# Optimization experiments

Hardware: AMD Instinct MI355X
Metric: run time of the kernel (lower is better)

## Reference

```python
import jax, jax.numpy as jnp
import numpy as np

D_MODEL = 128
NUM_LAYERS = 2
D_FF = 512
VOCAB = 128
OUT_DIM = 10
B, S = 512, 256
EPS_FEAT = 1e-6
LN_EPS = 1e-5


def _pos_encoding(seq_len, d):
    pos = jnp.arange(seq_len, dtype=jnp.float32)[:, None]            # [S,1]
    div = jnp.exp(jnp.arange(0, d, 2, dtype=jnp.float32) * (-np.log(10000.0) / d))
    ang = pos * div                                                   # [S,D/2]
    pe = jnp.stack([jnp.sin(ang), jnp.cos(ang)], axis=-1).reshape(seq_len, d)
    return pe[:, None, :]                                             # [S,1,D]


def _layer_norm(x, g, b):
    mu = jnp.mean(x, axis=-1, keepdims=True)
    var = jnp.mean(jnp.square(x - mu), axis=-1, keepdims=True)
    return (x - mu) * jax.lax.rsqrt(var + LN_EPS) * g + b


def setup_inputs() -> dict:
    key = jax.random.key(0)
    ks = jax.random.split(key, 20)
    sc = 0.02
    inp = {
        'src': jax.random.randint(ks[0], (B, S), 0, VOCAB),
        'emb': jax.random.normal(ks[1], (VOCAB, D_MODEL), jnp.float32) * sc,
        'wq': jax.random.normal(ks[2], (NUM_LAYERS, D_MODEL, D_MODEL), jnp.float32) * sc,
        'bq': jnp.zeros((NUM_LAYERS, D_MODEL), jnp.float32),
        'wk': jax.random.normal(ks[3], (NUM_LAYERS, D_MODEL, D_MODEL), jnp.float32) * sc,
        'bk': jnp.zeros((NUM_LAYERS, D_MODEL), jnp.float32),
        'wv': jax.random.normal(ks[4], (NUM_LAYERS, D_MODEL, D_MODEL), jnp.float32) * sc,
        'bv': jnp.zeros((NUM_LAYERS, D_MODEL), jnp.float32),
        'w1': jax.random.normal(ks[5], (NUM_LAYERS, D_FF, D_MODEL), jnp.float32) * sc,
        'b1': jnp.zeros((NUM_LAYERS, D_FF), jnp.float32),
        'w2': jax.random.normal(ks[6], (NUM_LAYERS, D_MODEL, D_FF), jnp.float32) * sc,
        'b2': jnp.zeros((NUM_LAYERS, D_MODEL), jnp.float32),
        'g1': jnp.ones((NUM_LAYERS, D_MODEL), jnp.float32),
        'beta1': jnp.zeros((NUM_LAYERS, D_MODEL), jnp.float32),
        'g2': jnp.ones((NUM_LAYERS, D_MODEL), jnp.float32),
        'beta2': jnp.zeros((NUM_LAYERS, D_MODEL), jnp.float32),
        'fc_w': jax.random.normal(ks[7], (OUT_DIM, D_MODEL), jnp.float32) * sc,
        'fc_b': jnp.zeros((OUT_DIM,), jnp.float32),
    }
    return inp


def reference(src, emb, wq, bq, wk, bk, wv, bv, w1, b1, w2, b2,
              g1, beta1, g2, beta2, fc_w, fc_b):
    # src: [B,S] int -> permute -> [S,B]
    x = emb[src.T] * np.sqrt(float(D_MODEL))          # [S,B,D]
    x = x + _pos_encoding(x.shape[0], D_MODEL)
    for l in range(NUM_LAYERS):
        # Linear attention (faithful to original: einsum 'b' axis = seq here)
        Q = jax.nn.relu(jnp.einsum('sbd,ed->sbe', x, wq[l]) + bq[l]) + EPS_FEAT
        K = jax.nn.relu(jnp.einsum('sbd,ed->sbe', x, wk[l]) + bk[l]) + EPS_FEAT
        V = jnp.einsum('sbd,ed->sbe', x, wv[l]) + bv[l]
        KV = jnp.einsum('snd,sne->sde', K, V)         # [S,D,D] (n = batch axis)
        Z = 1.0 / (jnp.einsum('snd,sd->sn', Q, K.sum(axis=1)) + EPS_FEAT)  # [S,B]
        attn = jnp.einsum('snd,sde,sn->sne', Q, KV, Z)  # [S,B,D]
        x = _layer_norm(x + attn, g1[l], beta1[l])
        ff = jnp.einsum('sbf,df->sbd',
                        jax.nn.relu(jnp.einsum('sbd,fd->sbf', x, w1[l]) + b1[l]),
                        w2[l]) + b2[l]
        x = _layer_norm(x + ff, g2[l], beta2[l])
    x = jnp.transpose(x, (1, 0, 2))                   # [B,S,D]
    pooled = jnp.mean(x, axis=1)                      # [B,D]
    return pooled @ fc_w.T + fc_b                     # [B,OUT]
```

## Files before the change

kernel.cpp:

```cpp
#include <hip/hip_runtime.h>

typedef unsigned short u16;
typedef unsigned int u32;
typedef short bf16x8 __attribute__((ext_vector_type(8)));
typedef float f32x4 __attribute__((ext_vector_type(4)));

__device__ __forceinline__ float b2f(u16 v) { return __uint_as_float(((u32)v) << 16); }
__device__ __forceinline__ u16 f2b(float f) {
    u32 x = __float_as_uint(f);
    return (u16)((x + 0x7fffu + ((x >> 16) & 1u)) >> 16);
}
__device__ __forceinline__ float lo16(u32 w) { return __uint_as_float(w << 16); }
__device__ __forceinline__ float hi16(u32 w) { return __uint_as_float(w & 0xffff0000u); }

#define S_LEN 256
#define B_SZ  512
#define DM    128
#define DFF   512
#define MROWS (S_LEN * B_SZ)

__device__ __forceinline__ int sw16(int r, int d) {
    return r * 128 + ((((d >> 3) ^ (r & 15)) & 15) << 3) + (d & 7);
}

__global__ __launch_bounds__(256) void detect_kernel(const u32* __restrict__ embw,
                                                     int* __restrict__ flag) {
    int z = 0, big = 0;
    for (int i = threadIdx.x; i < 8192; i += 256) {
        u32 w = embw[i];
        u32 lo = w & 0xffffu;
        if (lo == 0u) z++;
        else if (((lo >> 7) & 0xffu) >= 0xC0u) big++;
    }
#pragma unroll
    for (int off = 32; off > 0; off >>= 1) {
        z   += __shfl_xor(z, off, 64);
        big += __shfl_xor(big, off, 64);
    }
    __shared__ int zz[4], bb[4];
    if ((threadIdx.x & 63) == 0) { zz[threadIdx.x >> 6] = z; bb[threadIdx.x >> 6] = big; }
    __syncthreads();
    if (threadIdx.x == 0) {
        int Z = zz[0] + zz[1] + zz[2] + zz[3];
        int Bc = bb[0] + bb[1] + bb[2] + bb[3];
        flag[0] = (Z > 4096 || Bc > 16) ? 1 : 0;
    }
}

struct Ptrs { const void* p[17]; };

__global__ __launch_bounds__(256) void convert_kernel(Ptrs ps, u16* __restrict__ canon,
                                                      const int* __restrict__ flag) {
    const int cnt[17] = {16384,32768,256,32768,256,32768,256,131072,1024,131072,
                         256,256,256,256,256,1280,10};
    const int off[17] = {0,16384,49152,49408,82176,82432,115200,115456,246528,
                         247552,378624,378880,379136,379392,379648,379904,381184};
    const int bst[18] = {0,8,24,25,41,42,58,59,123,124,188,189,190,191,192,193,194,195};
    const int isf = *flag;
    const int blk = blockIdx.x;
    int idx = 0;
#pragma unroll
    for (int i = 0; i < 17; ++i) if (blk >= bst[i + 1]) idx = i + 1;
    const int local = blk - bst[idx];
    const int n = cnt[idx];
    const void* sp = ps.p[idx];
    u16* dp = canon + off[idx];
#pragma unroll
    for (int j = 0; j < 8; ++j) {
        int e = local * 2048 + j * 256 + threadIdx.x;
        if (e < n) {
            u16 v = isf ? f2b(((const float*)sp)[e]) : ((const u16*)sp)[e];
            dp[e] = v;
        }
    }
}

__global__ __launch_bounds__(256) void embed_kernel(const int* __restrict__ src,
                                                    const u16* __restrict__ emb,
                                                    u16* __restrict__ X) {
    int idx = blockIdx.x * 256 + threadIdx.x;
    int d2 = idx & 63;
    int m = idx >> 6;
    int s = m >> 9;
    int b = m & 511;
    int tok = src[b * S_LEN + s];
    int d = d2 * 2;
    float e0 = b2f(emb[tok * DM + d])     * 11.3137084989847604f;
    float e1 = b2f(emb[tok * DM + d + 1]) * 11.3137084989847604f;
    float ang = (float)s * expf((float)d * -0.0719557841560639f);
    float v0 = e0 + sinf(ang);
    float v1 = e1 + cosf(ang);
    u32 w = (u32)f2b(v0) | ((u32)f2b(v1) << 16);
    *(u32*)(X + (size_t)m * DM + d) = w;
}

__global__ __launch_bounds__(256) void kvproj_kernel(
    const u16* __restrict__ X, const u16* __restrict__ Wk, const u16* __restrict__ bk,
    const u16* __restrict__ Wv, const u16* __restrict__ bv,
    u16* __restrict__ KVt, float* __restrict__ Ksum)
{
    __shared__ __align__(16) char sm_[49152];
    u16* Xs = (u16*)sm_;
    u16* Kt = (u16*)(sm_ + 16384);
    u16* Vt = (u16*)(sm_ + 32768);
    const int s = blockIdx.x, t = threadIdx.x;
    const int w = t >> 6, quad = (t >> 4) & 3, lr = t & 15;
    const u16* Xg = X + (size_t)s * B_SZ * DM;

    bf16x8 wkf[2][4], wvf[2][4];
    float kb[2], vb[2];
#pragma unroll
    for (int ct = 0; ct < 2; ++ct) {
        int e = w * 32 + ct * 16 + lr;
#pragma unroll
        for (int kc = 0; kc < 4; ++kc) {
            wkf[ct][kc] = *(const bf16x8*)(Wk + e * 128 + kc * 32 + quad * 8);
            wvf[ct][kc] = *(const bf16x8*)(Wv + e * 128 + kc * 32 + quad * 8);
        }
        kb[ct] = b2f(bk[e]);
        vb[ct] = b2f(bv[e]);
    }

    const f32x4 z4 = {0.f, 0.f, 0.f, 0.f};
    f32x4 kvacc[2][8];
#pragma unroll
    for (int dt = 0; dt < 2; ++dt)
#pragma unroll
        for (int ct = 0; ct < 8; ++ct) kvacc[dt][ct] = z4;
    float ks[2] = {0.f, 0.f};

    for (int b0 = 0; b0 < B_SZ; b0 += 64) {
        __syncthreads();
#pragma unroll
        for (int i = 0; i < 4; ++i) {
            int e8 = (i * 256 + t) * 8; int r = e8 >> 7, k0 = e8 & 127;
            *(uint4*)(Xs + sw16(r, k0)) = *(const uint4*)(Xg + (size_t)(b0 + r) * DM + k0);
        }
        __syncthreads();
        f32x4 pa[4][2];
#pragma unroll
        for (int mt = 0; mt < 4; ++mt) { pa[mt][0] = z4; pa[mt][1] = z4; }
#pragma unroll
        for (int kc = 0; kc < 4; ++kc) {
            bf16x8 a[4];
#pragma unroll
            for (int mt = 0; mt < 4; ++mt)
                a[mt] = *(const bf16x8*)(Xs + sw16(mt * 16 + lr, kc * 32 + quad * 8));
#pragma unroll
            for (int ct = 0; ct < 2; ++ct)
#pragma unroll
                for (int mt = 0; mt < 4; ++mt)
                    pa[mt][ct] = __builtin_amdgcn_mfma_f32_16x16x32_bf16(a[mt], wkf[ct][kc], pa[mt][ct], 0, 0, 0);
        }
#pragma unroll
        for (int ct = 0; ct < 2; ++ct) {
            int e = w * 32 + ct * 16 + lr, e7 = e & 7;
#pragma unroll
            for (int mt = 0; mt < 4; ++mt) {
                u16 h[4]; float ssum = 0.f;
#pragma unroll
                for (int j = 0; j < 4; ++j) {
                    float v = fmaxf(pa[mt][ct][j] + kb[ct], 0.f) + 1e-6f;
                    h[j] = f2b(v); ssum += b2f(h[j]);
                }
                ks[ct] += ssum;
                uint2 pk; pk.x = (u32)h[0] | ((u32)h[1] << 16); pk.y = (u32)h[2] | ((u32)h[3] << 16);
                int bs = mt * 2 + (quad >> 1);
                *(uint2*)(Kt + e * 64 + (((bs ^ e7) & 7) << 3) + (quad & 1) * 4) = pk;
            }
        }
#pragma unroll
        for (int mt = 0; mt < 4; ++mt) { pa[mt][0] = z4; pa[mt][1] = z4; }
#pragma unroll
        for (int kc = 0; kc < 4; ++kc) {
            bf16x8 a[4];
#pragma unroll
            for (int mt = 0; mt < 4; ++mt)
                a[mt] = *(const bf16x8*)(Xs + sw16(mt * 16 + lr, kc * 32 + quad * 8));
#pragma unroll
            for (int ct = 0; ct < 2; ++ct)
#pragma unroll
                for (int mt = 0; mt < 4; ++mt)
                    pa[mt][ct] = __builtin_amdgcn_mfma_f32_16x16x32_bf16(a[mt], wvf[ct][kc], pa[mt][ct], 0, 0, 0);
        }
#pragma unroll
        for (int ct = 0; ct < 2; ++ct) {
            int e = w * 32 + ct * 16 + lr, e7 = e & 7;
#pragma unroll
            for (int mt = 0; mt < 4; ++mt) {
                u16 h[4];
#pragma unroll
                for (int j = 0; j < 4; ++j) h[j] = f2b(pa[mt][ct][j] + vb[ct]);
                uint2 pk; pk.x = (u32)h[0] | ((u32)h[1] << 16); pk.y = (u32)h[2] | ((u32)h[3] << 16);
                int bs = mt * 2 + (quad >> 1);
                *(uint2*)(Vt + e * 64 + (((bs ^ e7) & 7) << 3) + (quad & 1) * 4) = pk;
            }
        }
        __syncthreads();
#pragma unroll
        for (int kc = 0; kc < 2; ++kc) {
            bf16x8 ka[2];
#pragma unroll
            for (int dt = 0; dt < 2; ++dt) {
                int d = (2 * w + dt) * 16 + lr;
                ka[dt] = *(const bf16x8*)(Kt + d * 64 + ((((kc * 4 + quad) ^ (d & 7)) & 7) << 3));
            }
#pragma unroll
            for (int ct = 0; ct < 8; ++ct) {
                int e = ct * 16 + lr;
                bf16x8 vf = *(const bf16x8*)(Vt + e * 64 + ((((kc * 4 + quad) ^ (e & 7)) & 7) << 3));
                kvacc[0][ct] = __builtin_amdgcn_mfma_f32_16x16x32_bf16(ka[0], vf, kvacc[0][ct], 0, 0, 0);
                kvacc[1][ct] = __builtin_amdgcn_mfma_f32_16x16x32_bf16(ka[1], vf, kvacc[1][ct], 0, 0, 0);
            }
        }
    }
#pragma unroll
    for (int ct = 0; ct < 2; ++ct) {
        float v = ks[ct];
        v += __shfl_xor(v, 16, 64);
        v += __shfl_xor(v, 32, 64);
        if (quad == 0) Ksum[s * 128 + w * 32 + ct * 16 + lr] = v;
    }
    u16* KVg = KVt + (size_t)s * (DM * DM);
#pragma unroll
    for (int dt = 0; dt < 2; ++dt) {
        int d0 = (2 * w + dt) * 16 + quad * 4;
#pragma unroll
        for (int ct = 0; ct < 8; ++ct) {
            int e = ct * 16 + lr;
            u16 h[4];
#pragma unroll
            for (int j = 0; j < 4; ++j) h[j] = f2b(kvacc[dt][ct][j]);
            uint2 pk; pk.x = (u32)h[0] | ((u32)h[1] << 16); pk.y = (u32)h[2] | ((u32)h[3] << 16);
            *(uint2*)(KVg + e * 128 + d0) = pk;
        }
    }
}

__global__ __launch_bounds__(256) void attn_ln_kernel(
    const u16* X, const u16* __restrict__ Wq, const u16* __restrict__ bq,
    const u16* __restrict__ KVt, const float* __restrict__ Ksum,
    u16* Xout, const u16* __restrict__ g, const u16* __restrict__ beta)
{
    __shared__ __align__(16) char sm_[65536];
    u16* R1 = (u16*)sm_;
    u16* R2 = (u16*)(sm_ + 32768);
    const int blk = blockIdx.x, s = blk >> 2, rc = blk & 3, t = threadIdx.x;
    const int w = t >> 6, quad = (t >> 4) & 3, lr = t & 15;
    const size_t m0 = (size_t)s * B_SZ + rc * 128;

#pragma unroll
    for (int i = 0; i < 8; ++i) {
        int e8 = (i * 256 + t) * 8; int r = e8 >> 7, k0 = e8 & 127;
        *(uint4*)(R1 + sw16(r, k0)) = *(const uint4*)(Wq + e8);
        *(uint4*)(R2 + sw16(r, k0)) = *(const uint4*)(X + (m0 + r) * DM + k0);
    }
    __syncthreads();
    const f32x4 z4 = {0.f, 0.f, 0.f, 0.f};
    f32x4 qacc[2][8];
#pragma unroll
    for (int mt = 0; mt < 2; ++mt)
#pragma unroll
        for (int ct = 0; ct < 8; ++ct) qacc[mt][ct] = z4;
#pragma unroll
    for (int kc = 0; kc < 4; ++kc) {
        bf16x8 a[2];
#pragma unroll
        for (int mt = 0; mt < 2; ++mt)
            a[mt] = *(const bf16x8*)(R2 + sw16(w * 32 + mt * 16 + lr, kc * 32 + quad * 8));
#pragma unroll
        for (int ct = 0; ct < 8; ++ct) {
            bf16x8 wf = *(const bf16x8*)(R1 + sw16(ct * 16 + lr, kc * 32 + quad * 8));
            qacc[0][ct] = __builtin_amdgcn_mfma_f32_16x16x32_bf16(a[0], wf, qacc[0][ct], 0, 0, 0);
            qacc[1][ct] = __builtin_amdgcn_mfma_f32_16x16x32_bf16(a[1], wf, qacc[1][ct], 0, 0, 0);
        }
    }
    __syncthreads();
    float ksm[8], bqv[8];
#pragma unroll
    for (int ct = 0; ct < 8; ++ct) {
        ksm[ct] = Ksum[s * 128 + ct * 16 + lr];
        bqv[ct] = b2f(bq[ct * 16 + lr]);
    }
    float zden[2][4];
#pragma unroll
    for (int mt = 0; mt < 2; ++mt)
#pragma unroll
        for (int j = 0; j < 4; ++j) zden[mt][j] = 0.f;
#pragma unroll
    for (int mt = 0; mt < 2; ++mt)
#pragma unroll
        for (int ct = 0; ct < 8; ++ct) {
            int d = ct * 16 + lr;
#pragma unroll
            for (int j = 0; j < 4; ++j) {
                float qv = fmaxf(qacc[mt][ct][j] + bqv[ct], 0.f) + 1e-6f;
                u16 qb16 = f2b(qv);
                zden[mt][j] += b2f(qb16) * ksm[ct];
                int b = w * 32 + mt * 16 + quad * 4 + j;
                R1[sw16(b, d)] = qb16;
            }
        }
#pragma unroll
    for (int mt = 0; mt < 2; ++mt)
#pragma unroll
        for (int j = 0; j < 4; ++j) {
            float v = zden[mt][j];
            v += __shfl_xor(v, 1, 64); v += __shfl_xor(v, 2, 64);
            v += __shfl_xor(v, 4, 64); v += __shfl_xor(v, 8, 64);
            zden[mt][j] = 1.f / (v + 1e-6f);
        }
    const u16* KVg = KVt + (size_t)s * (DM * DM);
#pragma unroll
    for (int i = 0; i < 8; ++i) {
        int e8 = (i * 256 + t) * 8; int r = e8 >> 7, k0 = e8 & 127;
        *(uint4*)(R2 + sw16(r, k0)) = *(const uint4*)(KVg + e8);
    }
    __syncthreads();
    f32x4 oacc[2][8];
#pragma unroll
    for (int mt = 0; mt < 2; ++mt)
#pragma unroll
        for (int ct = 0; ct < 8; ++ct) oacc[mt][ct] = z4;
#pragma unroll
    for (int kc = 0; kc < 4; ++kc) {
        bf16x8 qa[2];
#pragma unroll
        for (int mt = 0; mt < 2; ++mt)
            qa[mt] = *(const bf16x8*)(R1 + sw16(w * 32 + mt * 16 + lr, kc * 32 + quad * 8));
#pragma unroll
        for (int ct = 0; ct < 8; ++ct) {
            bf16x8 kf = *(const bf16x8*)(R2 + sw16(ct * 16 + lr, kc * 32 + quad * 8));
            oacc[0][ct] = __builtin_amdgcn_mfma_f32_16x16x32_bf16(qa[0], kf, oacc[0][ct], 0, 0, 0);
            oacc[1][ct] = __builtin_amdgcn_mfma_f32_16x16x32_bf16(qa[1], kf, oacc[1][ct], 0, 0, 0);
        }
    }
    float gv[8], bev[8];
#pragma unroll
    for (int ct = 0; ct < 8; ++ct) {
        gv[ct]  = b2f(g[ct * 16 + lr]);
        bev[ct] = b2f(beta[ct * 16 + lr]);
    }
#pragma unroll
    for (int mt = 0; mt < 2; ++mt)
#pragma unroll
        for (int j = 0; j < 4; ++j) {
            int b = w * 32 + mt * 16 + quad * 4 + j;
            const u16* xr = X + (m0 + b) * DM;
            float vals[8], sum = 0.f, sq = 0.f;
#pragma unroll
            for (int ct = 0; ct < 8; ++ct) {
                float v = fmaf(oacc[mt][ct][j], zden[mt][j], b2f(xr[ct * 16 + lr]));
                vals[ct] = v; sum += v; sq += v * v;
            }
            sum += __shfl_xor(sum, 1, 64); sq += __shfl_xor(sq, 1, 64);
            sum += __shfl_xor(sum, 2, 64); sq += __shfl_xor(sq, 2, 64);
            sum += __shfl_xor(sum, 4, 64); sq += __shfl_xor(sq, 4, 64);
            sum += __shfl_xor(sum, 8, 64); sq += __shfl_xor(sq, 8, 64);
            float mean = sum * 0.0078125f;
            float var  = sq * 0.0078125f - mean * mean;
            float rstd = rsqrtf(fmaxf(var, 0.f) + 1e-5f);
            u16* xo = Xout + (m0 + b) * DM;
#pragma unroll
            for (int ct = 0; ct < 8; ++ct)
                xo[ct * 16 + lr] = f2b((vals[ct] - mean) * rstd * gv[ct] + bev[ct]);
        }
}

__global__ __launch_bounds__(256) void mlp_kernel(
    const u16* X, const u16* __restrict__ W1, const u16* __restrict__ b1,
    const u16* __restrict__ W2, const u16* __restrict__ b2,
    u16* Xout, const u16* __restrict__ g, const u16* __restrict__ beta)
{
    __shared__ __align__(16) char sm_[65536];
    u16* As  = (u16*)sm_;
    u16* W1c = (u16*)(sm_ + 32768);
    u16* Hc  = W1c;
    u16* W2c = (u16*)(sm_ + 49152);
    float* zs = (float*)sm_;
    const int t = threadIdx.x;
    const int m0 = blockIdx.x * 128;
    const int w  = t >> 6;
    const int lq = (t >> 4) & 3;
    const int lr = t & 15;

#pragma unroll
    for (int i = 0; i < 8; ++i) {
        int e = (i * 256 + t) * 8; int r = e >> 7, k0 = e & 127;
        *(uint4*)(As + sw16(r, k0)) = *(const uint4*)(X + (size_t)(m0 + r) * DM + k0);
    }

    const f32x4 zero4 = {0.f, 0.f, 0.f, 0.f};
    f32x4 zacc[2][8];
#pragma unroll
    for (int mt = 0; mt < 2; ++mt)
#pragma unroll
        for (int ct = 0; ct < 8; ++ct) zacc[mt][ct] = zero4;

    for (int fc = 0; fc < DFF; fc += 64) {
        __syncthreads();
#pragma unroll
        for (int i = 0; i < 4; ++i) {
            int e = (i * 256 + t) * 8; int c = e >> 7, k0 = e & 127;
            *(uint4*)(W1c + sw16(c, k0)) = *(const uint4*)(W1 + (size_t)(fc + c) * DM + k0);
        }
#pragma unroll
        for (int i = 0; i < 4; ++i) {
            int e = (i * 256 + t) * 8; int d = e >> 6, f0 = e & 63, sl = f0 >> 3;
            *(uint4*)(W2c + d * 64 + (((sl ^ (d & 7)) & 7) << 3)) =
                *(const uint4*)(W2 + (size_t)d * DFF + fc + f0);
        }
        __syncthreads();
        f32x4 hacc[2][4];
#pragma unroll
        for (int mt = 0; mt < 2; ++mt)
#pragma unroll
            for (int ct = 0; ct < 4; ++ct) hacc[mt][ct] = zero4;
#pragma unroll
        for (int kc = 0; kc < 4; ++kc) {
            bf16x8 af[2];
#pragma unroll
            for (int mt = 0; mt < 2; ++mt)
                af[mt] = *(const bf16x8*)(As + sw16(w * 32 + mt * 16 + lr, kc * 32 + lq * 8));
#pragma unroll
            for (int ct = 0; ct < 4; ++ct) {
                bf16x8 bf_ = *(const bf16x8*)(W1c + sw16(ct * 16 + lr, kc * 32 + lq * 8));
                hacc[0][ct] = __builtin_amdgcn_mfma_f32_16x16x32_bf16(af[0], bf_, hacc[0][ct], 0, 0, 0);
                hacc[1][ct] = __builtin_amdgcn_mfma_f32_16x16x32_bf16(af[1], bf_, hacc[1][ct], 0, 0, 0);
            }
        }
        __syncthreads();
#pragma unroll
        for (int ct = 0; ct < 4; ++ct) {
            int f = ct * 16 + lr;
            float hbv = b2f(b1[fc + f]);
#pragma unroll
            for (int mt = 0; mt < 2; ++mt)
#pragma unroll
                for (int j = 0; j < 4; ++j) {
                    int m = w * 32 + mt * 16 + lq * 4 + j;
                    float v = fmaxf(hacc[mt][ct][j] + hbv, 0.f);
                    Hc[m * 64 + ((((f >> 3) ^ (m & 7)) & 7) << 3) + (f & 7)] = f2b(v);
                }
        }
        __syncthreads();
#pragma unroll
        for (int kc = 0; kc < 2; ++kc) {
            bf16x8 ha[2];
#pragma unroll
            for (int mt = 0; mt < 2; ++mt) {
                int m = w * 32 + mt * 16 + lr;
                ha[mt] = *(const bf16x8*)(Hc + m * 64 + ((((kc * 4 + lq) ^ (lr & 7)) & 7) << 3));
            }
#pragma unroll
            for (int ct = 0; ct < 8; ++ct) {
                int d = ct * 16 + lr;
                bf16x8 wb = *(const bf16x8*)(W2c + d * 64 + ((((kc * 4 + lq) ^ (lr & 7)) & 7) << 3));
                zacc[0][ct] = __builtin_amdgcn_mfma_f32_16x16x32_bf16(ha[0], wb, zacc[0][ct], 0, 0, 0);
                zacc[1][ct] = __builtin_amdgcn_mfma_f32_16x16x32_bf16(ha[1], wb, zacc[1][ct], 0, 0, 0);
            }
        }
    }
    __syncthreads();
#pragma unroll
    for (int ct = 0; ct < 8; ++ct) {
        float bbv = b2f(b2[ct * 16 + lr]);
#pragma unroll
        for (int mt = 0; mt < 2; ++mt)
#pragma unroll
            for (int j = 0; j < 4; ++j) {
                int r = w * 32 + mt * 16 + lq * 4 + j;
                zs[r * 128 + ct * 16 + lr] = zacc[mt][ct][j] + bbv;
            }
    }
    __syncthreads();
    int wv = t >> 6, ln = t & 63;
    float g0 = b2f(g[ln]), g1v = b2f(g[64 + ln]);
    float be0 = b2f(beta[ln]), be1 = b2f(beta[64 + ln]);
    for (int q = 0; q < 32; ++q) {
        int r = wv * 32 + q;
        float v0 = zs[r * 128 + ln]      + b2f(X[(size_t)(m0 + r) * DM + ln]);
        float v1 = zs[r * 128 + 64 + ln] + b2f(X[(size_t)(m0 + r) * DM + 64 + ln]);
        float sum = v0 + v1, sq = v0 * v0 + v1 * v1;
#pragma unroll
        for (int off = 32; off > 0; off >>= 1) {
            sum += __shfl_xor(sum, off, 64);
            sq  += __shfl_xor(sq,  off, 64);
        }
        float mean = sum * 0.0078125f;
        float var  = sq * 0.0078125f - mean * mean;
        float rstd = rsqrtf(fmaxf(var, 0.f) + 1e-5f);
        Xout[(size_t)(m0 + r) * DM + ln]      = f2b((v0 - mean) * rstd * g0  + be0);
        Xout[(size_t)(m0 + r) * DM + 64 + ln] = f2b((v1 - mean) * rstd * g1v + be1);
    }
}

__global__ __launch_bounds__(128) void pool_fc_kernel(
    const u16* __restrict__ X, const u16* __restrict__ fcw,
    const u16* __restrict__ fcb, void* __restrict__ Out,
    const int* __restrict__ flag)
{
    __shared__ float pool[128];
    const int b = blockIdx.x, t = threadIdx.x;
    float acc = 0.f;
    for (int s = 0; s < S_LEN; ++s)
        acc += b2f(X[((size_t)s * B_SZ + b) * DM + t]);
    pool[t] = acc * (1.0f / 256.0f);
    __syncthreads();
    if (t < 10) {
        float o = b2f(fcb[t]);
        for (int d = 0; d < 128; ++d) o += pool[d] * b2f(fcw[t * 128 + d]);
        if (*flag) ((float*)Out)[b * 10 + t] = o;
        else       ((u16*)Out)[b * 10 + t] = f2b(o);
    }
}

extern "C" void kernel_launch(void* const* d_in, const int* in_sizes, int n_in,
                              void* d_out, int out_size, void* d_ws, size_t ws_size,
                              hipStream_t stream)
{
    const int* src = (const int*)d_in[0];

    char* ws = (char*)d_ws;
    u16*   X    = (u16*)ws;
    u16*   KVt  = (u16*)(ws + 33554432);
    float* Ksum = (float*)(ws + 41943040);
    int*   flag = (int*)(ws + 42074112);
    u16*   cn   = (u16*)(ws + 42074368);

    u16* emb = cn + 0;
    u16* wq  = cn + 16384;
    u16* bq  = cn + 49152;
    u16* wk  = cn + 49408;
    u16* bk  = cn + 82176;
    u16* wv  = cn + 82432;
    u16* bvp = cn + 115200;
    u16* w1  = cn + 115456;
    u16* b1  = cn + 246528;
    u16* w2  = cn + 247552;
    u16* b2  = cn + 378624;
    u16* g1  = cn + 378880;
    u16* be1 = cn + 379136;
    u16* g2  = cn + 379392;
    u16* be2 = cn + 379648;
    u16* fcw = cn + 379904;
    u16* fcb = cn + 381184;

    detect_kernel<<<1, 256, 0, stream>>>((const u32*)d_in[1], flag);

    Ptrs ps;
    for (int i = 0; i < 17; ++i) ps.p[i] = d_in[i + 1];
    convert_kernel<<<195, 256, 0, stream>>>(ps, cn, flag);

    embed_kernel<<<MROWS * 64 / 256, 256, 0, stream>>>(src, emb, X);

    for (int l = 0; l < 2; ++l) {
        kvproj_kernel<<<S_LEN, 256, 0, stream>>>(
            X, wk + l * DM * DM, bk + l * DM, wv + l * DM * DM, bvp + l * DM, KVt, Ksum);
        attn_ln_kernel<<<S_LEN * 4, 256, 0, stream>>>(
            X, wq + l * DM * DM, bq + l * DM, KVt, Ksum, X, g1 + l * DM, be1 + l * DM);
        mlp_kernel<<<MROWS / 128, 256, 0, stream>>>(
            X, w1 + l * DFF * DM, b1 + l * DFF, w2 + l * DM * DFF, b2 + l * DM,
            X, g2 + l * DM, be2 + l * DM);
    }

    pool_fc_kernel<<<B_SZ, 128, 0, stream>>>(X, fcw, fcb, d_out, flag);
}
```

Baseline: 448.2 us.

## Restructure MLP kernel: register-resident X fragments, smaller LDS, in-register LayerNorm

The MLP kernel now keeps each wave's X rows as bf16 MFMA fragments in registers instead of staging them in a 32KB shared tile. It also swaps the MFMA operand order so H comes out row-major per lane, which allows packed 8-byte H stores and drops two barriers per chunk, since each wave only touches its own rows of H. The final bias, residual and LayerNorm run straight from the accumulators using 16-lane shuffles, removing the fp32 shared staging. LDS drops from 64KB to 48KB and launch bounds ask for 3 blocks per CU, trading extra register pressure for occupancy.

```diff
diff --git a/kernel.cpp b/kernel.cpp
--- a/kernel.cpp
+++ b/kernel.cpp
@@ -367,47 +367,44 @@
         }
 }
 
-__global__ __launch_bounds__(256) void mlp_kernel(
+__global__ __launch_bounds__(256, 3) void mlp_kernel(
     const u16* X, const u16* __restrict__ W1, const u16* __restrict__ b1,
     const u16* __restrict__ W2, const u16* __restrict__ b2,
     u16* Xout, const u16* __restrict__ g, const u16* __restrict__ beta)
 {
-    __shared__ __align__(16) char sm_[65536];
-    u16* As  = (u16*)sm_;
-    u16* W1c = (u16*)(sm_ + 32768);
-    u16* Hc  = W1c;
-    u16* W2c = (u16*)(sm_ + 49152);
-    float* zs = (float*)sm_;
+    __shared__ __align__(16) u16 W1c[64 * 128];
+    __shared__ __align__(16) u16 W2c[128 * 64];
+    __shared__ __align__(16) u16 Hc[128 * 64];
     const int t = threadIdx.x;
     const int m0 = blockIdx.x * 128;
-    const int w  = t >> 6;
-    const int lq = (t >> 4) & 3;
-    const int lr = t & 15;
-
-#pragma unroll
-    for (int i = 0; i < 8; ++i) {
-        int e = (i * 256 + t) * 8; int r = e >> 7, k0 = e & 127;
-        *(uint4*)(As + sw16(r, k0)) = *(const uint4*)(X + (size_t)(m0 + r) * DM + k0);
-    }
-
-    const f32x4 zero4 = {0.f, 0.f, 0.f, 0.f};
+    const int w = t >> 6, quad = (t >> 4) & 3, lr = t & 15;
+
+    bf16x8 xf[2][4];
+#pragma unroll
+    for (int mt = 0; mt < 2; ++mt)
+#pragma unroll
+        for (int kc = 0; kc < 4; ++kc)
+            xf[mt][kc] = *(const bf16x8*)(X + (size_t)(m0 + w * 32 + mt * 16 + lr) * DM
+                                            + kc * 32 + quad * 8);
+
+    const f32x4 z4 = {0.f, 0.f, 0.f, 0.f};
     f32x4 zacc[2][8];
 #pragma unroll
     for (int mt = 0; mt < 2; ++mt)
 #pragma unroll
-        for (int ct = 0; ct < 8; ++ct) zacc[mt][ct] = zero4;
+        for (int ct = 0; ct < 8; ++ct) zacc[mt][ct] = z4;
 
     for (int fc = 0; fc < DFF; fc += 64) {
         __syncthreads();
 #pragma unroll
         for (int i = 0; i < 4; ++i) {
-            int e = (i * 256 + t) * 8; int c = e >> 7, k0 = e & 127;
-            *(uint4*)(W1c + sw16(c, k0)) = *(const uint4*)(W1 + (size_t)(fc + c) * DM + k0);
+            int e8 = (i * 256 + t) * 8; int r = e8 >> 7, k0 = e8 & 127;
+            *(uint4*)(W1c + sw16(r, k0)) = *(const uint4*)(W1 + (size_t)(fc + r) * DM + k0);
         }
 #pragma unroll
         for (int i = 0; i < 4; ++i) {
-            int e = (i * 256 + t) * 8; int d = e >> 6, f0 = e & 63, sl = f0 >> 3;
-            *(uint4*)(W2c + d * 64 + (((sl ^ (d & 7)) & 7) << 3)) =
+            int e8 = (i * 256 + t) * 8; int d = e8 >> 6, f0 = e8 & 63;
+            *(uint4*)(W2c + d * 64 + ((((f0 >> 3) ^ (d & 7)) & 7) << 3)) =
                 *(const uint4*)(W2 + (size_t)d * DFF + fc + f0);
         }
         __syncthreads();
@@ -415,84 +412,82 @@
 #pragma unroll
         for (int mt = 0; mt < 2; ++mt)
 #pragma unroll
-            for (int ct = 0; ct < 4; ++ct) hacc[mt][ct] = zero4;
+            for (int ct = 0; ct < 4; ++ct) hacc[mt][ct] = z4;
 #pragma unroll
         for (int kc = 0; kc < 4; ++kc) {
-            bf16x8 af[2];
-#pragma unroll
-            for (int mt = 0; mt < 2; ++mt)
-                af[mt] = *(const bf16x8*)(As + sw16(w * 32 + mt * 16 + lr, kc * 32 + lq * 8));
 #pragma unroll
             for (int ct = 0; ct < 4; ++ct) {
-                bf16x8 bf_ = *(const bf16x8*)(W1c + sw16(ct * 16 + lr, kc * 32 + lq * 8));
-                hacc[0][ct] = __builtin_amdgcn_mfma_f32_16x16x32_bf16(af[0], bf_, hacc[0][ct], 0, 0, 0);
-                hacc[1][ct] = __builtin_amdgcn_mfma_f32_16x16x32_bf16(af[1], bf_, hacc[1][ct], 0, 0, 0);
-            }
-        }
-        __syncthreads();
+                bf16x8 wa = *(const bf16x8*)(W1c + sw16(ct * 16 + lr, kc * 32 + quad * 8));
+                hacc[0][ct] = __builtin_amdgcn_mfma_f32_16x16x32_bf16(wa, xf[0][kc], hacc[0][ct], 0, 0, 0);
+                hacc[1][ct] = __builtin_amdgcn_mfma_f32_16x16x32_bf16(wa, xf[1][kc], hacc[1][ct], 0, 0, 0);
+            }
+        }
 #pragma unroll
         for (int ct = 0; ct < 4; ++ct) {
-            int f = ct * 16 + lr;
-            float hbv = b2f(b1[fc + f]);
-#pragma unroll
-            for (int mt = 0; mt < 2; ++mt)
-#pragma unroll
-                for (int j = 0; j < 4; ++j) {
-                    int m = w * 32 + mt * 16 + lq * 4 + j;
-                    float v = fmaxf(hacc[mt][ct][j] + hbv, 0.f);
-                    Hc[m * 64 + ((((f >> 3) ^ (m & 7)) & 7) << 3) + (f & 7)] = f2b(v);
-                }
-        }
-        __syncthreads();
+            float hb[4];
+#pragma unroll
+            for (int j = 0; j < 4; ++j) hb[j] = b2f(b1[fc + ct * 16 + quad * 4 + j]);
+#pragma unroll
+            for (int mt = 0; mt < 2; ++mt) {
+                int m = w * 32 + mt * 16 + lr;
+                u16 h[4];
+#pragma unroll
+                for (int j = 0; j < 4; ++j)
+                    h[j] = f2b(fmaxf(hacc[mt][ct][j] + hb[j], 0.f));
+                uint2 pk; pk.x = (u32)h[0] | ((u32)h[1] << 16);
+                pk.y = (u32)h[2] | ((u32)h[3] << 16);
+                int slot = (ct * 2 + (quad >> 1)) ^ (m & 7);
+                *(uint2*)(Hc + m * 64 + (slot << 3) + (quad & 1) * 4) = pk;
+            }
+        }
 #pragma unroll
         for (int kc = 0; kc < 2; ++kc) {
             bf16x8 ha[2];
 #pragma unroll
             for (int mt = 0; mt < 2; ++mt) {
                 int m = w * 32 + mt * 16 + lr;
-                ha[mt] = *(const bf16x8*)(Hc + m * 64 + ((((kc * 4 + lq) ^ (lr & 7)) & 7) << 3));
+                ha[mt] = *(const bf16x8*)(Hc + m * 64 + ((((kc * 4 + quad) ^ (m & 7)) & 7) << 3));
             }
 #pragma unroll
             for (int ct = 0; ct < 8; ++ct) {
                 int d = ct * 16 + lr;
-                bf16x8 wb = *(const bf16x8*)(W2c + d * 64 + ((((kc * 4 + lq) ^ (lr & 7)) & 7) << 3));
+                bf16x8 wb = *(const bf16x8*)(W2c + d * 64 + ((((kc * 4 + quad) ^ (d & 7)) & 7) << 3));
                 zacc[0][ct] = __builtin_amdgcn_mfma_f32_16x16x32_bf16(ha[0], wb, zacc[0][ct], 0, 0, 0);
                 zacc[1][ct] = __builtin_amdgcn_mfma_f32_16x16x32_bf16(ha[1], wb, zacc[1][ct], 0, 0, 0);
             }
         }
     }
-    __syncthreads();
+    float gv[8], bev[8], b2v[8];
 #pragma unroll
     for (int ct = 0; ct < 8; ++ct) {
-        float bbv = b2f(b2[ct * 16 + lr]);
-#pragma unroll
-        for (int mt = 0; mt < 2; ++mt)
-#pragma unroll
-            for (int j = 0; j < 4; ++j) {
-                int r = w * 32 + mt * 16 + lq * 4 + j;
-                zs[r * 128 + ct * 16 + lr] = zacc[mt][ct][j] + bbv;
-            }
-    }
-    __syncthreads();
-    int wv = t >> 6, ln = t & 63;
-    float g0 = b2f(g[ln]), g1v = b2f(g[64 + ln]);
-    float be0 = b2f(beta[ln]), be1 = b2f(beta[64 + ln]);
-    for (int q = 0; q < 32; ++q) {
-        int r = wv * 32 + q;
-        float v0 = zs[r * 128 + ln]      + b2f(X[(size_t)(m0 + r) * DM + ln]);
-        float v1 = zs[r * 128 + 64 + ln] + b2f(X[(size_t)(m0 + r) * DM + 64 + ln]);
-        float sum = v0 + v1, sq = v0 * v0 + v1 * v1;
-#pragma unroll
-        for (int off = 32; off > 0; off >>= 1) {
-            sum += __shfl_xor(sum, off, 64);
-            sq  += __shfl_xor(sq,  off, 64);
-        }
-        float mean = sum * 0.0078125f;
-        float var  = sq * 0.0078125f - mean * mean;
-        float rstd = rsqrtf(fmaxf(var, 0.f) + 1e-5f);
-        Xout[(size_t)(m0 + r) * DM + ln]      = f2b((v0 - mean) * rstd * g0  + be0);
-        Xout[(size_t)(m0 + r) * DM + 64 + ln] = f2b((v1 - mean) * rstd * g1v + be1);
-    }
+        gv[ct]  = b2f(g[ct * 16 + lr]);
+        bev[ct] = b2f(beta[ct * 16 + lr]);
+        b2v[ct] = b2f(b2[ct * 16 + lr]);
+    }
+#pragma unroll
+    for (int mt = 0; mt < 2; ++mt)
+#pragma unroll
+        for (int j = 0; j < 4; ++j) {
+            int r = w * 32 + mt * 16 + quad * 4 + j;
+            const u16* xr = X + (size_t)(m0 + r) * DM;
+            float vals[8], sum = 0.f, sq = 0.f;
+#pragma unroll
+            for (int ct = 0; ct < 8; ++ct) {
+                float v = zacc[mt][ct][j] + b2v[ct] + b2f(xr[ct * 16 + lr]);
+                vals[ct] = v; sum += v; sq += v * v;
+            }
+            sum += __shfl_xor(sum, 1, 64); sq += __shfl_xor(sq, 1, 64);
+            sum += __shfl_xor(sum, 2, 64); sq += __shfl_xor(sq, 2, 64);
+            sum += __shfl_xor(sum, 4, 64); sq += __shfl_xor(sq, 4, 64);
+            sum += __shfl_xor(sum, 8, 64); sq += __shfl_xor(sq, 8, 64);
+            float mean = sum * 0.0078125f;
+            float var  = sq * 0.0078125f - mean * mean;
+            float rstd = rsqrtf(fmaxf(var, 0.f) + 1e-5f);
+            u16* xo = Xout + (size_t)(m0 + r) * DM;
+#pragma unroll
+            for (int ct = 0; ct < 8; ++ct)
+                xo[ct * 16 + lr] = f2b((vals[ct] - mean) * rstd * gv[ct] + bev[ct]);
+        }
 }
 
 __global__ __launch_bounds__(128) void pool_fc_kernel(
```

After: 462.1 us. 3.1% more time.
